# Kernel tuning notes

Hardware: AMD Instinct MI355X
Metric: run time of the kernel (lower is better)

## Reference

```python
import jax, jax.numpy as jnp
import numpy as np

B, S, E, H = 4, 2048, 2048, 16
D = E // H  # head_dim = 128


def _rotary_tables():
    # standard interleaved RoPE: pairs (2i, 2i+1) share an angle
    inv_freq = 1.0 / (10000.0 ** (np.arange(0, D, 2, dtype=np.float64) / D))
    ang = np.arange(S, dtype=np.float64)[:, None] * inv_freq[None, :]  # [S, D/2]
    ang = np.repeat(ang, 2, axis=-1)  # [S, D]
    cos = np.cos(ang).astype(np.float32)[None, None]  # [1,1,S,D]
    sin = np.sin(ang).astype(np.float32)[None, None]
    return jnp.asarray(cos), jnp.asarray(sin)


def setup_inputs() -> dict:
    key = jax.random.key(0)
    ks = jax.random.split(key, 4)
    x = jax.random.normal(ks[0], (B, S, E), jnp.float32)
    cos, sin = _rotary_tables()
    Wqkv = jax.random.normal(ks[1], (E, 3 * E), jnp.float32) * 0.02
    bqkv = jnp.zeros((3 * E,), jnp.float32)
    Wproj = jax.random.normal(ks[2], (E, E), jnp.float32) * 0.02
    bproj = jnp.zeros((E,), jnp.float32)
    return {"x": x, "rotary_cos": cos, "rotary_sin": sin,
            "Wqkv": Wqkv, "bqkv": bqkv, "Wproj": Wproj, "bproj": bproj}


def apply_rotary(t, cos, sin):
    # t: [B,H,S,D]; interleaved rotate-half: (x1,x2) -> (-x2, x1)
    x1 = t[..., 0::2]
    x2 = t[..., 1::2]
    rot = jnp.stack((-x2, x1), axis=-1).reshape(t.shape)
    return t * cos + rot * sin


def reference(x, rotary_cos, rotary_sin, Wqkv, bqkv, Wproj, bproj):
    qkv = x @ Wqkv + bqkv  # [B,S,3E]
    q, k, v = jnp.split(qkv, 3, axis=-1)
    # [B,S,E] -> [B,H,S,D]
    to_heads = lambda t: t.reshape(B, S, H, D).transpose(0, 2, 1, 3)
    q, k, v = to_heads(q), to_heads(k), to_heads(v)
    q = apply_rotary(q, rotary_cos, rotary_sin)
    k = apply_rotary(k, rotary_cos, rotary_sin)
    scale = 1.0 / jnp.sqrt(jnp.float32(D))
    scores = jnp.einsum("bhqd,bhkd->bhqk", q, k) * scale  # non-causal
    attn = jax.nn.softmax(scores, axis=-1)
    y = jnp.einsum("bhqk,bhkd->bhqd", attn, v)
    y = y.transpose(0, 2, 1, 3).reshape(B, S, E)
    out = y @ Wproj + bproj
    return out, k, v
```

## Files before the change

kernel.cpp:

```cpp
#include <hip/hip_runtime.h>


typedef unsigned short u16;
typedef unsigned int   u32;
typedef float  f32x4  __attribute__((ext_vector_type(4)));
typedef __bf16 bf16x8 __attribute__((ext_vector_type(8)));

#define B_  4
#define S_  2048
#define E_  2048
#define H_  16
#define D_  128

__device__ __forceinline__ u16 f2bf(float f) {
    union { float f; u32 u; } v; v.f = f;
    return (u16)((v.u + 0x8000u) >> 16);
}
__device__ __forceinline__ u32 pack_bf(float a, float b) {
    union { float f; u32 u; } x, y; x.f = a; y.f = b;
    return ((x.u + 0x8000u) >> 16) | ((y.u + 0x8000u) & 0xFFFF0000u);
}
__device__ __forceinline__ float bf2f(u16 h) {
    union { u32 u; float f; } v; v.u = ((u32)h) << 16; return v.f;
}

__device__ __forceinline__ void gld16(const u16* g, u16* l) {
    __builtin_amdgcn_global_load_lds(
        (const __attribute__((address_space(1))) void*)g,
        (__attribute__((address_space(3))) void*)l, 16, 0, 0);
}

__global__ __launch_bounds__(256) void xconv_kernel(
    const float* __restrict__ x, u16* __restrict__ xb)
{
    size_t g = (size_t)blockIdx.x * 256 + threadIdx.x;
    const float4* p = (const float4*)x + g * 2;
    float4 a = p[0], b = p[1];
    uint4 pk;
    pk.x = pack_bf(a.x, a.y); pk.y = pack_bf(a.z, a.w);
    pk.z = pack_bf(b.x, b.y); pk.w = pack_bf(b.z, b.w);
    ((uint4*)xb)[g] = pk;
}

__global__ __launch_bounds__(256) void wtrans_kernel(
    const float* __restrict__ W, u16* __restrict__ WT, int K, int N)
{
    __shared__ float tile[64][65];
    const int n0 = blockIdx.x * 64, k0 = blockIdx.y * 64;
    const int t = threadIdx.x;
#pragma unroll
    for (int i = 0; i < 16; ++i) {
        int idx = i * 256 + t; int r = idx >> 6, c = idx & 63;
        tile[r][c] = W[(size_t)(k0 + r) * N + n0 + c];
    }
    __syncthreads();
#pragma unroll
    for (int i = 0; i < 16; ++i) {
        int idx = i * 256 + t; int rn = idx >> 6, ck = idx & 63;
        WT[(size_t)(n0 + rn) * K + k0 + ck] = f2bf(tile[ck][rn]);
    }
}

template <int MODE>
__global__ __launch_bounds__(256) void gemm_kernel(
    const u16* __restrict__ A, const u16* __restrict__ Bt,
    const float* __restrict__ bias,
    u16* __restrict__ qh, u16* __restrict__ kh, u16* __restrict__ vt,
    float* __restrict__ vout, float* __restrict__ outf,
    int N, int K)
{
    __shared__ u16 As[128 * 32];
    __shared__ u16 Bs[128 * 32];

    const int t = threadIdx.x;
    const int wave = t >> 6, lane = t & 63, quad = lane >> 4, l16 = lane & 15;
    const int wr = wave >> 1, wc = wave & 1;
    const int m0 = blockIdx.y * 128, n0 = blockIdx.x * 128;

    f32x4 acc[4][4] = {};
    const int swr = (quad ^ ((l16 >> 1) & 3)) << 3;

    for (int k0 = 0; k0 < K; k0 += 32) {
        __syncthreads();
#pragma unroll
        for (int i = 0; i < 2; ++i) {
            int idx = i * 256 + t;
            int row = idx >> 2, c = (idx & 3) ^ ((row >> 1) & 3);
            gld16(A  + (size_t)(m0 + row) * K + k0 + (c << 3),
                  As + ((i * 256 + wave * 64) << 3));
            gld16(Bt + (size_t)(n0 + row) * K + k0 + (c << 3),
                  Bs + ((i * 256 + wave * 64) << 3));
        }
        __syncthreads();

        bf16x8 af[4], bfr[4];
#pragma unroll
        for (int mi = 0; mi < 4; ++mi)
            af[mi] = *(const bf16x8*)(As + (wr * 64 + mi * 16 + l16) * 32 + swr);
#pragma unroll
        for (int ni = 0; ni < 4; ++ni)
            bfr[ni] = *(const bf16x8*)(Bs + (wc * 64 + ni * 16 + l16) * 32 + swr);
#pragma unroll
        for (int mi = 0; mi < 4; ++mi)
#pragma unroll
            for (int ni = 0; ni < 4; ++ni)
                acc[mi][ni] = __builtin_amdgcn_mfma_f32_16x16x32_bf16(
                    af[mi], bfr[ni], acc[mi][ni], 0, 0, 0);
    }

    if constexpr (MODE == 0) {
        const int sel = n0 >> 11;
        const int h   = (n0 & 2047) >> 7;
        const int b   = m0 >> 11, sb = m0 & 2047;
        const size_t hb = ((size_t)(b * H_ + h)) * S_ * D_;
#pragma unroll
        for (int mi = 0; mi < 4; ++mi) {
            int s0 = sb + wr * 64 + mi * 16 + quad * 4;
#pragma unroll
            for (int ni = 0; ni < 4; ++ni) {
                int d = wc * 64 + ni * 16 + l16;
                float bv = bias[n0 + d];
                float v0 = acc[mi][ni][0] + bv, v1 = acc[mi][ni][1] + bv;
                float v2 = acc[mi][ni][2] + bv, v3 = acc[mi][ni][3] + bv;
                size_t base = hb + (size_t)s0 * D_ + d;
                if (sel < 2) {
                    u16* dst = sel ? kh : qh;
                    dst[base]        = f2bf(v0); dst[base + D_]    = f2bf(v1);
                    dst[base + 2*D_] = f2bf(v2); dst[base + 3*D_]  = f2bf(v3);
                } else {
                    vout[base] = v0; vout[base + D_] = v1;
                    vout[base + 2*D_] = v2; vout[base + 3*D_] = v3;
                    uint2 pk; pk.x = pack_bf(v0, v1); pk.y = pack_bf(v2, v3);
                    *(uint2*)(vt + ((size_t)(b * H_ + h) * D_ + d) * S_ + s0) = pk;
                }
            }
        }
    } else {
#pragma unroll
        for (int mi = 0; mi < 4; ++mi) {
            int row0 = m0 + wr * 64 + mi * 16 + quad * 4;
#pragma unroll
            for (int ni = 0; ni < 4; ++ni) {
                int col = n0 + wc * 64 + ni * 16 + l16;
                float bv = bias[col];
#pragma unroll
                for (int r = 0; r < 4; ++r)
                    outf[(size_t)(row0 + r) * N + col] = acc[mi][ni][r] + bv;
            }
        }
    }
}

__global__ __launch_bounds__(256) void rotary_kernel(
    u16* __restrict__ q, u16* __restrict__ k, float* __restrict__ kout,
    const float* __restrict__ cosT, const float* __restrict__ sinT)
{
    const int g = blockIdx.x * 256 + threadIdx.x;
    const int d0 = (g & 15) << 3;
    const int srow = g >> 4;
    const int s = srow & (S_ - 1);
    const size_t base = (size_t)srow * D_ + d0;

    uint4 qv = *(const uint4*)(q + base);
    uint4 kv = *(const uint4*)(k + base);
    float cc[8], ss[8];
    *(float4*)(cc)     = *(const float4*)(cosT + s * D_ + d0);
    *(float4*)(cc + 4) = *(const float4*)(cosT + s * D_ + d0 + 4);
    *(float4*)(ss)     = *(const float4*)(sinT + s * D_ + d0);
    *(float4*)(ss + 4) = *(const float4*)(sinT + s * D_ + d0 + 4);
    const u16* qp = (const u16*)&qv; const u16* kp = (const u16*)&kv;
    float qo[8], ko[8];
#pragma unroll
    for (int i = 0; i < 4; ++i) {
        float q1 = bf2f(qp[2*i]), q2 = bf2f(qp[2*i+1]);
        float k1 = bf2f(kp[2*i]), k2 = bf2f(kp[2*i+1]);
        qo[2*i]   = q1 * cc[2*i]   - q2 * ss[2*i];
        qo[2*i+1] = q2 * cc[2*i+1] + q1 * ss[2*i+1];
        ko[2*i]   = k1 * cc[2*i]   - k2 * ss[2*i];
        ko[2*i+1] = k2 * cc[2*i+1] + k1 * ss[2*i+1];
    }
    const float qs_ = 0.08838834764831845f * 1.4426950408889634f;
    uint4 qpk, kpk;
    u32* qq = (u32*)&qpk; u32* kq = (u32*)&kpk;
#pragma unroll
    for (int i = 0; i < 4; ++i) {
        qq[i] = pack_bf(qo[2*i] * qs_, qo[2*i+1] * qs_);
        kq[i] = pack_bf(ko[2*i], ko[2*i+1]);
    }
    *(uint4*)(q + base) = qpk;
    *(uint4*)(k + base) = kpk;
    *(float4*)(kout + base)     = make_float4(ko[0], ko[1], ko[2], ko[3]);
    *(float4*)(kout + base + 4) = make_float4(ko[4], ko[5], ko[6], ko[7]);
}

#define KSWZ(row, c) ((row) * 128 + (((c) ^ ((row) & 7)) << 3))
#define VSWZ(d, c)   ((d) * 64 + (((c) ^ ((d) & 7)) << 3))
#define PSWZ(qr, c)  ((qr) * 64 + (((c) ^ ((qr) & 7)) << 3))

__global__ __launch_bounds__(256, 4) void attn_kernel(
    const u16* __restrict__ qh, const u16* __restrict__ kh,
    const u16* __restrict__ vt, u16* __restrict__ yb)
{
    __shared__ u16 Ks[64 * 128];
    __shared__ u16 Vs[128 * 64];
    __shared__ u16 Ps[4 * 16 * 64];

    const int t = threadIdx.x, wave = t >> 6, lane = t & 63;
    const int quad = lane >> 4, l16 = lane & 15;
    const int bh = blockIdx.y, q0 = blockIdx.x * 64;
    const u16* kb = kh + (size_t)bh * S_ * D_;
    const u16* vb = vt + (size_t)bh * D_ * S_;
    u16* Pw = Ps + wave * (16 * 64);

    bf16x8 qf[4];
    {
        const u16* qp = qh + ((size_t)bh * S_ + q0 + wave * 16 + l16) * D_ + quad * 8;
#pragma unroll
        for (int kk = 0; kk < 4; ++kk) qf[kk] = *(const bf16x8*)(qp + kk * 32);
    }

    f32x4 o[8] = {};
    float m_r = -1e30f, l_r = 0.f;

    for (int k0 = 0; k0 < S_; k0 += 64) {
        __syncthreads();
#pragma unroll
        for (int i = 0; i < 4; ++i) {
            int idx = i * 256 + t;
            {
                int row = idx >> 4, c = (idx & 15) ^ (row & 7);
                gld16(kb + (size_t)(k0 + row) * D_ + (c << 3),
                      Ks + ((i * 256 + wave * 64) << 3));
            }
            {
                int d = idx >> 3, c = (idx & 7) ^ (d & 7);
                gld16(vb + (size_t)d * S_ + k0 + (c << 3),
                      Vs + ((i * 256 + wave * 64) << 3));
            }
        }
        __syncthreads();

        f32x4 sc[4] = {};
#pragma unroll
        for (int kk = 0; kk < 4; ++kk) {
#pragma unroll
            for (int nt = 0; nt < 4; ++nt) {
                bf16x8 kf = *(const bf16x8*)(Ks + KSWZ(nt * 16 + l16, kk * 4 + quad));
                sc[nt] = __builtin_amdgcn_mfma_f32_16x16x32_bf16(kf, qf[kk], sc[nt], 0, 0, 0);
            }
        }
        float mx = sc[0][0];
#pragma unroll
        for (int nt = 0; nt < 4; ++nt)
#pragma unroll
            for (int r = 0; r < 4; ++r) mx = fmaxf(mx, sc[nt][r]);
        mx = fmaxf(mx, __shfl_xor(mx, 16));
        mx = fmaxf(mx, __shfl_xor(mx, 32));
        float mn = fmaxf(m_r, mx);
        float alpha = exp2f(m_r - mn);
        m_r = mn;
        float rs = 0.f;
#pragma unroll
        for (int nt = 0; nt < 4; ++nt)
#pragma unroll
            for (int r = 0; r < 4; ++r) {
                float p = exp2f(sc[nt][r] - mn);
                sc[nt][r] = p; rs += p;
            }
        rs += __shfl_xor(rs, 16);
        rs += __shfl_xor(rs, 32);
        l_r = l_r * alpha + rs;
        float af4[4];
#pragma unroll
        for (int r = 0; r < 4; ++r) af4[r] = __shfl(alpha, quad * 4 + r);
#pragma unroll
        for (int dt = 0; dt < 8; ++dt)
#pragma unroll
            for (int r = 0; r < 4; ++r) o[dt][r] *= af4[r];

#pragma unroll
        for (int nt = 0; nt < 4; ++nt) {
            int key0 = nt * 16 + quad * 4;
            int chunk = key0 >> 3, sub = key0 & 7;
            uint2 pk;
            pk.x = pack_bf(sc[nt][0], sc[nt][1]);
            pk.y = pack_bf(sc[nt][2], sc[nt][3]);
            *(uint2*)(Pw + PSWZ(l16, chunk) + sub) = pk;
        }
#pragma unroll
        for (int kk2 = 0; kk2 < 2; ++kk2) {
            bf16x8 pf = *(const bf16x8*)(Pw + PSWZ(l16, kk2 * 4 + quad));
#pragma unroll
            for (int dt = 0; dt < 8; ++dt) {
                bf16x8 vf = *(const bf16x8*)(Vs + VSWZ(dt * 16 + l16, kk2 * 4 + quad));
                o[dt] = __builtin_amdgcn_mfma_f32_16x16x32_bf16(pf, vf, o[dt], 0, 0, 0);
            }
        }
    }
    float lf[4];
#pragma unroll
    for (int r = 0; r < 4; ++r) {
        float lv = __shfl(l_r, quad * 4 + r);
        lf[r] = __builtin_amdgcn_rcpf(lv);
    }
    const int b = bh >> 4, h = bh & 15;
#pragma unroll
    for (int dt = 0; dt < 8; ++dt) {
        int d = h * D_ + dt * 16 + l16;
#pragma unroll
        for (int r = 0; r < 4; ++r) {
            int s = q0 + wave * 16 + quad * 4 + r;
            yb[(size_t)(b * S_ + s) * E_ + d] = f2bf(o[dt][r] * lf[r]);
        }
    }
}

extern "C" void kernel_launch(void* const* d_in, const int* in_sizes, int n_in,
                              void* d_out, int out_size, void* d_ws, size_t ws_size,
                              hipStream_t stream)
{
    (void)in_sizes; (void)n_in; (void)out_size; (void)ws_size;
    const float* x     = (const float*)d_in[0];
    const float* cosT  = (const float*)d_in[1];
    const float* sinT  = (const float*)d_in[2];
    const float* Wqkv  = (const float*)d_in[3];
    const float* bqkv  = (const float*)d_in[4];
    const float* Wproj = (const float*)d_in[5];
    const float* bproj = (const float*)d_in[6];

    float* out  = (float*)d_out;
    float* kout = out  + (size_t)B_ * S_ * E_;
    float* vout = kout + (size_t)B_ * S_ * E_;

    u16* wqkvT  = (u16*)d_ws;
    u16* wprojT = wqkvT  + (size_t)12582912;
    u16* qh     = wprojT + (size_t)4194304;
    u16* kh     = qh     + (size_t)16777216;
    u16* vt     = kh     + (size_t)16777216;
    u16* yb     = vt     + (size_t)16777216;
    u16* xb     = yb;

    xconv_kernel<<<8192, 256, 0, stream>>>(x, xb);
    wtrans_kernel<<<dim3(96, 32), 256, 0, stream>>>(Wqkv, wqkvT, 2048, 6144);
    wtrans_kernel<<<dim3(32, 32), 256, 0, stream>>>(Wproj, wprojT, 2048, 2048);
    gemm_kernel<0><<<dim3(48, 64), 256, 0, stream>>>(
        xb, wqkvT, bqkv, qh, kh, vt, vout, nullptr, 6144, 2048);
    rotary_kernel<<<8192, 256, 0, stream>>>(qh, kh, kout, cosT, sinT);
    attn_kernel<<<dim3(32, 64), 256, 0, stream>>>(qh, kh, vt, yb);
    gemm_kernel<1><<<dim3(16, 64), 256, 0, stream>>>(
        yb, wprojT, bproj, nullptr, nullptr, nullptr, nullptr, out, 2048, 2048);
}
```

Before: 898.1 us.

## Restructure GEMM into 256x256 tiles with double-buffered LDS and phased MFMA scheduling

Both GEMM kernels now use 256x256 tiles with 512 threads and a K step of 64. A and B halves are staged into double-buffered LDS while the MFMA phases run, with explicit waitcnt, barriers and setprio around each phase, and the LDS layout uses an XOR swizzle over 8 chunks. This is meant to hide global-load latency and raise MFMA density per LDS read. In exchange it needs much more LDS (128KB per block) and registers for acc[8][4], and the grid becomes small (768 and 256 blocks), which risks poor occupancy and wave quantization on the projection GEMM.

```diff
diff --git a/kernel.cpp b/kernel.cpp
--- a/kernel.cpp
+++ b/kernel.cpp
@@ -61,65 +61,141 @@
     }
 }
 
+__device__ __forceinline__ void stage_half(
+    const u16* __restrict__ g, int K, u16* l, int t)
+{
+    const int wb = (t >> 6) << 6;
+#pragma unroll
+    for (int j = 0; j < 2; ++j) {
+        const int idx = j * 512 + t;
+        const int row = idx >> 3, c = (idx & 7) ^ (row & 7);
+        gld16(g + (size_t)row * K + (c << 3),
+              l + ((j * 512 + wb) << 3));
+    }
+}
+
 template <int MODE>
-__global__ __launch_bounds__(256) void gemm_kernel(
+__global__ __launch_bounds__(512, 2) void gemm_kernel(
     const u16* __restrict__ A, const u16* __restrict__ Bt,
     const float* __restrict__ bias,
     u16* __restrict__ qh, u16* __restrict__ kh, u16* __restrict__ vt,
     float* __restrict__ vout, float* __restrict__ outf,
     int N, int K)
 {
-    __shared__ u16 As[128 * 32];
-    __shared__ u16 Bs[128 * 32];
+    __shared__ u16 Asm[2][256 * 64];
+    __shared__ u16 Bsm[2][256 * 64];
 
     const int t = threadIdx.x;
     const int wave = t >> 6, lane = t & 63, quad = lane >> 4, l16 = lane & 15;
-    const int wr = wave >> 1, wc = wave & 1;
-    const int m0 = blockIdx.y * 128, n0 = blockIdx.x * 128;
-
-    f32x4 acc[4][4] = {};
-    const int swr = (quad ^ ((l16 >> 1) & 3)) << 3;
-
-    for (int k0 = 0; k0 < K; k0 += 32) {
-        __syncthreads();
-#pragma unroll
-        for (int i = 0; i < 2; ++i) {
-            int idx = i * 256 + t;
-            int row = idx >> 2, c = (idx & 3) ^ ((row >> 1) & 3);
-            gld16(A  + (size_t)(m0 + row) * K + k0 + (c << 3),
-                  As + ((i * 256 + wave * 64) << 3));
-            gld16(Bt + (size_t)(n0 + row) * K + k0 + (c << 3),
-                  Bs + ((i * 256 + wave * 64) << 3));
-        }
-        __syncthreads();
-
-        bf16x8 af[4], bfr[4];
-#pragma unroll
-        for (int mi = 0; mi < 4; ++mi)
-            af[mi] = *(const bf16x8*)(As + (wr * 64 + mi * 16 + l16) * 32 + swr);
-#pragma unroll
-        for (int ni = 0; ni < 4; ++ni)
-            bfr[ni] = *(const bf16x8*)(Bs + (wc * 64 + ni * 16 + l16) * 32 + swr);
-#pragma unroll
-        for (int mi = 0; mi < 4; ++mi)
-#pragma unroll
-            for (int ni = 0; ni < 4; ++ni)
-                acc[mi][ni] = __builtin_amdgcn_mfma_f32_16x16x32_bf16(
-                    af[mi], bfr[ni], acc[mi][ni], 0, 0, 0);
+    const int wr = wave >> 2, wc = wave & 3;
+    const int m0 = blockIdx.y * 256, n0 = blockIdx.x * 256;
+    const int NT = K >> 6;
+
+    const int sw0 = ((quad ^ (l16 & 7)) << 3);
+    const int sw1 = (((4 + quad) ^ (l16 & 7)) << 3);
+    const int aRow = (wr * 128 + l16) << 6;
+    const int bRow = (wc * 64 + l16) << 6;
+
+    f32x4 acc[8][4] = {};
+
+    const u16* Ab = A  + (size_t)m0 * K;
+    const u16* Bb = Bt + (size_t)n0 * K;
+
+    stage_half(Ab,                        K, &Asm[0][0],    t);
+    stage_half(Ab + (size_t)128 * K,      K, &Asm[0][8192], t);
+    stage_half(Bb,                        K, &Bsm[0][0],    t);
+    stage_half(Bb + (size_t)128 * K,      K, &Bsm[0][8192], t);
+    stage_half(Ab + 64,                   K, &Asm[1][0],    t);
+    stage_half(Ab + (size_t)128 * K + 64, K, &Asm[1][8192], t);
+    asm volatile("s_waitcnt vmcnt(4)" ::: "memory");
+    __builtin_amdgcn_s_barrier();
+
+    for (int T = 0; T < NT; ++T) {
+        const int cur = T & 1, nxt = cur ^ 1;
+        const int kn1 = (T + 1) << 6, kn2 = (T + 2) << 6;
+        const u16* Asb = &Asm[cur][0];
+        const u16* Bsb = &Bsm[cur][0];
+        bf16x8 af[8], b0, b1;
+
+#pragma unroll
+        for (int mi = 0; mi < 8; ++mi)
+            af[mi] = *(const bf16x8*)(Asb + aRow + mi * 1024 + sw0);
+        b0 = *(const bf16x8*)(Bsb + bRow + sw0);
+        b1 = *(const bf16x8*)(Bsb + bRow + 1024 + sw0);
+        if (T + 1 < NT) stage_half(Bb + kn1, K, &Bsm[nxt][0], t);
+        __builtin_amdgcn_s_barrier();
+        asm volatile("s_waitcnt lgkmcnt(0)" ::: "memory");
+        __builtin_amdgcn_s_setprio(1);
+#pragma unroll
+        for (int mi = 0; mi < 8; ++mi) {
+            acc[mi][0] = __builtin_amdgcn_mfma_f32_16x16x32_bf16(af[mi], b0, acc[mi][0], 0, 0, 0);
+            acc[mi][1] = __builtin_amdgcn_mfma_f32_16x16x32_bf16(af[mi], b1, acc[mi][1], 0, 0, 0);
+        }
+        __builtin_amdgcn_s_setprio(0);
+        __builtin_amdgcn_s_barrier();
+
+        b0 = *(const bf16x8*)(Bsb + bRow + 2048 + sw0);
+        b1 = *(const bf16x8*)(Bsb + bRow + 3072 + sw0);
+        if (T + 1 < NT) stage_half(Bb + (size_t)128 * K + kn1, K, &Bsm[nxt][8192], t);
+        __builtin_amdgcn_s_barrier();
+        asm volatile("s_waitcnt lgkmcnt(0)" ::: "memory");
+        __builtin_amdgcn_s_setprio(1);
+#pragma unroll
+        for (int mi = 0; mi < 8; ++mi) {
+            acc[mi][2] = __builtin_amdgcn_mfma_f32_16x16x32_bf16(af[mi], b0, acc[mi][2], 0, 0, 0);
+            acc[mi][3] = __builtin_amdgcn_mfma_f32_16x16x32_bf16(af[mi], b1, acc[mi][3], 0, 0, 0);
+        }
+        __builtin_amdgcn_s_setprio(0);
+        __builtin_amdgcn_s_barrier();
+
+#pragma unroll
+        for (int mi = 0; mi < 8; ++mi)
+            af[mi] = *(const bf16x8*)(Asb + aRow + mi * 1024 + sw1);
+        b0 = *(const bf16x8*)(Bsb + bRow + sw1);
+        b1 = *(const bf16x8*)(Bsb + bRow + 1024 + sw1);
+        __builtin_amdgcn_s_barrier();
+        asm volatile("s_waitcnt lgkmcnt(0)" ::: "memory");
+        __builtin_amdgcn_s_setprio(1);
+#pragma unroll
+        for (int mi = 0; mi < 8; ++mi) {
+            acc[mi][0] = __builtin_amdgcn_mfma_f32_16x16x32_bf16(af[mi], b0, acc[mi][0], 0, 0, 0);
+            acc[mi][1] = __builtin_amdgcn_mfma_f32_16x16x32_bf16(af[mi], b1, acc[mi][1], 0, 0, 0);
+        }
+        __builtin_amdgcn_s_setprio(0);
+        __builtin_amdgcn_s_barrier();
+
+        b0 = *(const bf16x8*)(Bsb + bRow + 2048 + sw1);
+        b1 = *(const bf16x8*)(Bsb + bRow + 3072 + sw1);
+        if (T + 2 < NT) {
+            stage_half(Ab + kn2,                   K, &Asm[cur][0],    t);
+            stage_half(Ab + (size_t)128 * K + kn2, K, &Asm[cur][8192], t);
+        }
+        __builtin_amdgcn_s_barrier();
+        asm volatile("s_waitcnt lgkmcnt(0)" ::: "memory");
+        __builtin_amdgcn_s_setprio(1);
+#pragma unroll
+        for (int mi = 0; mi < 8; ++mi) {
+            acc[mi][2] = __builtin_amdgcn_mfma_f32_16x16x32_bf16(af[mi], b0, acc[mi][2], 0, 0, 0);
+            acc[mi][3] = __builtin_amdgcn_mfma_f32_16x16x32_bf16(af[mi], b1, acc[mi][3], 0, 0, 0);
+        }
+        __builtin_amdgcn_s_setprio(0);
+        if (T + 2 < NT) { asm volatile("s_waitcnt vmcnt(4)" ::: "memory"); }
+        else            { asm volatile("s_waitcnt vmcnt(0)" ::: "memory"); }
+        __builtin_amdgcn_s_barrier();
     }
 
     if constexpr (MODE == 0) {
         const int sel = n0 >> 11;
-        const int h   = (n0 & 2047) >> 7;
         const int b   = m0 >> 11, sb = m0 & 2047;
-        const size_t hb = ((size_t)(b * H_ + h)) * S_ * D_;
-#pragma unroll
-        for (int mi = 0; mi < 4; ++mi) {
-            int s0 = sb + wr * 64 + mi * 16 + quad * 4;
-#pragma unroll
-            for (int ni = 0; ni < 4; ++ni) {
-                int d = wc * 64 + ni * 16 + l16;
-                float bv = bias[n0 + d];
+#pragma unroll
+        for (int ni = 0; ni < 4; ++ni) {
+            const int dg = (n0 & 2047) + wc * 64 + ni * 16 + l16;
+            const int h = dg >> 7, d = dg & 127;
+            const float bv = bias[n0 + wc * 64 + ni * 16 + l16];
+            const size_t hb = ((size_t)(b * H_ + h)) * S_ * D_;
+#pragma unroll
+            for (int mi = 0; mi < 8; ++mi) {
+                const int s0 = sb + wr * 128 + mi * 16 + quad * 4;
                 float v0 = acc[mi][ni][0] + bv, v1 = acc[mi][ni][1] + bv;
                 float v2 = acc[mi][ni][2] + bv, v3 = acc[mi][ni][3] + bv;
                 size_t base = hb + (size_t)s0 * D_ + d;
@@ -137,12 +213,12 @@
         }
     } else {
 #pragma unroll
-        for (int mi = 0; mi < 4; ++mi) {
-            int row0 = m0 + wr * 64 + mi * 16 + quad * 4;
-#pragma unroll
-            for (int ni = 0; ni < 4; ++ni) {
-                int col = n0 + wc * 64 + ni * 16 + l16;
-                float bv = bias[col];
+        for (int ni = 0; ni < 4; ++ni) {
+            const int col = n0 + wc * 64 + ni * 16 + l16;
+            const float bv = bias[col];
+#pragma unroll
+            for (int mi = 0; mi < 8; ++mi) {
+                const int row0 = m0 + wr * 128 + mi * 16 + quad * 4;
 #pragma unroll
                 for (int r = 0; r < 4; ++r)
                     outf[(size_t)(row0 + r) * N + col] = acc[mi][ni][r] + bv;
@@ -343,10 +419,10 @@
     xconv_kernel<<<8192, 256, 0, stream>>>(x, xb);
     wtrans_kernel<<<dim3(96, 32), 256, 0, stream>>>(Wqkv, wqkvT, 2048, 6144);
     wtrans_kernel<<<dim3(32, 32), 256, 0, stream>>>(Wproj, wprojT, 2048, 2048);
-    gemm_kernel<0><<<dim3(48, 64), 256, 0, stream>>>(
+    gemm_kernel<0><<<dim3(24, 32), 512, 0, stream>>>(
         xb, wqkvT, bqkv, qh, kh, vt, vout, nullptr, 6144, 2048);
     rotary_kernel<<<8192, 256, 0, stream>>>(qh, kh, kout, cosT, sinT);
     attn_kernel<<<dim3(32, 64), 256, 0, stream>>>(qh, kh, vt, yb);
-    gemm_kernel<1><<<dim3(16, 64), 256, 0, stream>>>(
+    gemm_kernel<1><<<dim3(8, 32), 512, 0, stream>>>(
         yb, wprojT, bproj, nullptr, nullptr, nullptr, nullptr, out, 2048, 2048);
 }
```

Result: faster. 843.9 us (-6.0%).
